# Kernel tuning notes

Measured on AMD Instinct MI355X. Metric: run time of the kernel, lower is better.

The kernel has to match this reference:

```python
import jax, jax.numpy as jnp
import numpy as np
from jax import lax

EMB, HDIM, OBS_LEN = 64, 64, 8
BATCH, NSCENES, SCENE = 32768, 4096, 8
SEQ_LEN = 12


def setup_inputs() -> dict:
    key = jax.random.key(0)
    ks = jax.random.split(key, 16)
    obs_traj = jax.random.normal(ks[0], (OBS_LEN, BATCH, 2), jnp.float32)
    last_pos = jax.random.normal(ks[1], (BATCH, 2), jnp.float32)
    last_pos_rel = jax.random.normal(ks[2], (BATCH, 2), jnp.float32)
    starts = jnp.arange(NSCENES, dtype=jnp.int32) * SCENE
    seq_start_end = jnp.stack([starts, starts + SCENE], axis=1)  # (NSCENES, 2)
    # spatial_embedding: Linear(2, EMB)
    W_se = jax.random.normal(ks[3], (EMB, 2), jnp.float32) * 0.5
    b_se = jax.random.normal(ks[4], (EMB,), jnp.float32) * 0.1
    # weight-normed convs: w = g * v / ||v||_(in,k) per out-channel, bias init zero
    def conv_params(k, cout, cin, ksz):
        ka, kb = jax.random.split(k)
        std = np.sqrt(4.0 / (ksz * cin))
        v = jax.random.normal(ka, (cout, cin, ksz), jnp.float32) * std
        g = jax.random.uniform(kb, (cout,), jnp.float32, 0.5, 1.5)
        b = jnp.zeros((cout,), jnp.float32)
        return v, g, b
    v1, g1, b1 = conv_params(ks[5], HDIM, EMB, 3)
    v2, g2, b2 = conv_params(ks[6], HDIM // 2, HDIM, 3)
    v3, g3, b3 = conv_params(ks[7], HDIM // 2, HDIM // 2, 3)
    # hidden2pos: Linear(2*HDIM, 2)
    W_hp = jax.random.normal(ks[8], (2, 2 * HDIM), jnp.float32) * 0.05
    b_hp = jax.random.normal(ks[9], (2,), jnp.float32) * 0.05
    return {"obs_traj": obs_traj, "last_pos": last_pos, "last_pos_rel": last_pos_rel,
            "W_se": W_se, "b_se": b_se,
            "v1": v1, "g1": g1, "b1": b1,
            "v2": v2, "g2": g2, "b2": b2,
            "v3": v3, "g3": g3, "b3": b3,
            "W_hp": W_hp, "b_hp": b_hp,
            "seq_start_end": seq_start_end, "seq_len": SEQ_LEN}


def _wn_conv_relu(x, v, g, b):
    # weight-norm: w[o] = g[o] * v[o] / ||v[o]||  (norm over in-channels and kernel)
    norm = jnp.sqrt(jnp.sum(v * v, axis=(1, 2)))
    w = v * (g / norm)[:, None, None]
    y = lax.conv_general_dilated(x, w, (1,), 'VALID',
                                 dimension_numbers=('NCH', 'OIH', 'NCH'))
    return jax.nn.relu(y + b[None, :, None])


def reference(obs_traj, last_pos, last_pos_rel,
              W_se, b_se, v1, g1, b1, v2, g2, b2, v3, g3, b3, W_hp, b_hp,
              seq_start_end, seq_len):
    batch = last_pos.shape[0]
    nseg = seq_start_end.shape[0]
    h_dim = v1.shape[0]
    # scene id for each pedestrian (segments are contiguous [start,end) ranges)
    seg = jnp.searchsorted(seq_start_end[:, 0], jnp.arange(batch), side='right') - 1
    # obs_traj embedding -> (batch, EMB, OBS_LEN)
    emb = obs_traj @ W_se.T + b_se            # (T, B, EMB)
    obs_emb0 = jnp.transpose(emb, (1, 2, 0))  # (B, EMB, T)

    def step(carry, _):
        obs_emb, lp = carry
        s = _wn_conv_relu(obs_emb, v1, g1, b1)   # (B, H, T-2)
        s = _wn_conv_relu(s, v2, g2, b2)         # (B, H/2, T-4)
        s = _wn_conv_relu(s, v3, g3, b3)         # (B, H/2, T-6)
        s = s.reshape(batch, h_dim)              # (H/2)*(T-6) == H
        mx = jax.ops.segment_max(s, seg, num_segments=nseg)  # ragged per-scene max
        st = jnp.concatenate([s, mx[seg]], axis=1)           # (B, 2H)
        rel = st @ W_hp.T + b_hp                 # (B, 2)
        lp = rel + lp
        dec = rel @ W_se.T + b_se                # (B, EMB)
        obs_emb = jnp.concatenate([obs_emb[:, :, 1:], dec[:, :, None]], axis=2)
        return (obs_emb, lp), rel

    _, rels = lax.scan(step, (obs_emb0, last_pos), None, length=seq_len)
    return rels  # (seq_len, batch, 2)
```

## Files before the change

kernel.cpp:

```cpp
#include <hip/hip_runtime.h>

#define BATCH 32768
#define SEQLEN 12
#define NBLK 512

typedef short short8 __attribute__((ext_vector_type(8)));
typedef float f32x4 __attribute__((ext_vector_type(4)));
typedef unsigned short ushort_t;

static __device__ __forceinline__ unsigned short f2bf(float x) {
    unsigned u = __float_as_uint(x);
    return (unsigned short)((u + 0x7FFFu + ((u >> 16) & 1u)) >> 16);
}
static __device__ __forceinline__ float bf2f(unsigned short h) {
    return __uint_as_float(((unsigned)h) << 16);
}

#define MFMA __builtin_amdgcn_mfma_f32_16x16x32_bf16


#define C1PED(PX, PY, QX, QY, RX, RY, PPED) do {                              \
    float v_ = cK1;                                                           \
    v_ = fmaf(ccA0, PX, v_); v_ = fmaf(ccB0, PY, v_);                         \
    v_ = fmaf(ccA1, QX, v_); v_ = fmaf(ccB1, QY, v_);                         \
    v_ = fmaf(ccA2, RX, v_); v_ = fmaf(ccB2, RY, v_);                         \
    v_ = fmaxf(v_, 0.f);                                                      \
    ushort_t h_ = f2bf(v_);                                                   \
    s1sh[wv][PPED][lane] = h_;                                                \
    s1sl[wv][PPED][lane] = f2bf(v_ - bf2f(h_));                               \
} while(0)

#define S1_FRAGREAD(SL) do {                                                  \
    s1fh[SL][0] = *(const short8*)&s1sh[wv][n][kg*8];                         \
    s1fh[SL][1] = *(const short8*)&s1sh[wv][n][32 + kg*8];                    \
    s1fl[SL][0] = *(const short8*)&s1sl[wv][n][kg*8];                         \
    s1fl[SL][1] = *(const short8*)&s1sl[wv][n][32 + kg*8];                    \
} while(0)

#define CONV1COL(SA, SB, SC, SL) do {                                         \
    _Pragma("unroll")                                                         \
    for (int pp_ = 0; pp_ < 8; ++pp_) {                                       \
        float4 fa_ = *(const float4*)&pos_s[wv][SA][2*pp_][0];                \
        float4 fb_ = *(const float4*)&pos_s[wv][SB][2*pp_][0];                \
        float4 fc_ = *(const float4*)&pos_s[wv][SC][2*pp_][0];                \
        C1PED(fa_.x, fa_.y, fb_.x, fb_.y, fc_.x, fc_.y, 2*pp_);               \
        C1PED(fa_.z, fa_.w, fb_.z, fb_.w, fc_.z, fc_.w, 2*pp_+1);             \
    }                                                                         \
    S1_FRAGREAD(SL);                                                          \
} while(0)

#define CONV2COL(CM3) do {                                                    \
    const float* b2b_ = &b2s[0];                                              \
    asm volatile("" : "+v"(b2b_));                                            \
    _Pragma("unroll")                                                         \
    for (int T = 0; T < 2; ++T) {                                             \
        f32x4 a1 = {0.f,0.f,0.f,0.f}, a2 = {0.f,0.f,0.f,0.f},                 \
              a3 = {0.f,0.f,0.f,0.f};                                         \
        _Pragma("unroll")                                                     \
        for (int kb = 0; kb < 6; ++kb) {                                      \
            const int sl = ((CM3) + (kb >> 1)) % 3, ich = kb & 1;             \
            const short8 wh = *(const short8*)&c2wh[T*6+kb][lane][0];         \
            const short8 wl = *(const short8*)&c2wl[T*6+kb][lane][0];         \
            a1 = MFMA(wh, s1fh[sl][ich], a1, 0, 0, 0);                        \
            a2 = MFMA(wh, s1fl[sl][ich], a2, 0, 0, 0);                        \
            a3 = MFMA(wl, s1fh[sl][ich], a3, 0, 0, 0);                        \
        }                                                                     \
        const float4 bb = *(const float4*)&b2b_[T*16 + kg*4];                 \
        float w0 = fmaxf(a1[0]+a2[0]+a3[0]+bb.x, 0.f);                        \
        float w1 = fmaxf(a1[1]+a2[1]+a3[1]+bb.y, 0.f);                        \
        float w2 = fmaxf(a1[2]+a2[2]+a3[2]+bb.z, 0.f);                        \
        float w3 = fmaxf(a1[3]+a2[3]+a3[3]+bb.w, 0.f);                        \
        ushort_t h0=f2bf(w0), h1=f2bf(w1), h2=f2bf(w2), h3=f2bf(w3);          \
        *(uint2*)&s2sh[wv][n][T*16 + kg*4] = make_uint2(                      \
            (unsigned)h0 | ((unsigned)h1 << 16),                              \
            (unsigned)h2 | ((unsigned)h3 << 16));                             \
        *(uint2*)&s2sl[wv][n][T*16 + kg*4] = make_uint2(                      \
            (unsigned)f2bf(w0-bf2f(h0)) | ((unsigned)f2bf(w1-bf2f(h1)) << 16),\
            (unsigned)f2bf(w2-bf2f(h2)) | ((unsigned)f2bf(w3-bf2f(h3)) << 16));\
    }                                                                         \
    s2fh[(CM3)] = *(const short8*)&s2sh[wv][n][kg*8];                         \
    s2fl[(CM3)] = *(const short8*)&s2sl[wv][n][kg*8];                         \
} while(0)

#define CONV3COL(VM3, PARI) do {                                              \
    const float* b3b_ = &b3s[0];                                              \
    asm volatile("" : "+v"(b3b_));                                            \
    _Pragma("unroll")                                                         \
    for (int T = 0; T < 2; ++T) {                                             \
        f32x4 a1 = {0.f,0.f,0.f,0.f}, a2 = {0.f,0.f,0.f,0.f},                 \
              a3 = {0.f,0.f,0.f,0.f};                                         \
        _Pragma("unroll")                                                     \
        for (int kb = 0; kb < 3; ++kb) {                                      \
            const int sl = ((VM3) + kb) % 3;                                  \
            const short8 wh = *(const short8*)&c3wh[T*3+kb][lane][0];         \
            a1 = MFMA(wh, s2fh[sl], a1, 0, 0, 0);                             \
            a2 = MFMA(wh, s2fl[sl], a2, 0, 0, 0);                             \
            a3 = MFMA(c3l[T][kb], s2fh[sl], a3, 0, 0, 0);                     \
        }                                                                     \
        const float4 b3v = *(const float4*)&b3b_[T*16 + kg*4];                \
        float m0 = fmaxf(a1[0]+a2[0]+a3[0]+b3v.x, 0.f);                       \
        float m1 = fmaxf(a1[1]+a2[1]+a3[1]+b3v.y, 0.f);                       \
        float m2 = fmaxf(a1[2]+a2[2]+a3[2]+b3v.z, 0.f);                       \
        float m3 = fmaxf(a1[3]+a2[3]+a3[3]+b3v.w, 0.f);                       \
        c3c[PARI][T] = (f32x4){m0, m1, m2, m3};                               \
        _Pragma("unroll")                                                     \
        for (int msk = 1; msk <= 4; msk <<= 1) {                              \
            m0 = fmaxf(m0, __shfl_xor(m0, msk));                              \
            m1 = fmaxf(m1, __shfl_xor(m1, msk));                              \
            m2 = fmaxf(m2, __shfl_xor(m2, msk));                              \
            m3 = fmaxf(m3, __shfl_xor(m3, msk));                              \
        }                                                                     \
        mxc[PARI][T] = (f32x4){m0, m1, m2, m3};                               \
    }                                                                         \
} while(0)

#define STAGE2(T0) do {                                                       \
    const int tau_ = (T0) + (lane >> 5);                                      \
    const int p_ = (lane >> 1) & 15, c_ = lane & 1;                           \
    pos_s[wv][tau_ & 3][p_][c_] =                                             \
        obs[(size_t)(tau_*BATCH + bped + p_)*2 + c_];                         \
} while(0)

#define STEP(K) do {                                                          \
    const int st = sbase + (K);                                               \
    float pv0a = 0.f, pv0b = 0.f, pv1a = 0.f, pv1b = 0.f;                     \
    {                                                                         \
        const float* wqf_ = &whp_s[kg][0];                                    \
        asm volatile("" : "+v"(wqf_));     \
        const float4* wq = (const float4*)wqf_;                               \
        _Pragma("unroll")                                                     \
        for (int q = 0; q < 16; ++q) {                                        \
            float4 ww = wq[q];                                                \
            _Pragma("unroll")                                                 \
            for (int e = 0; e < 4; ++e) {                                     \
                const int j2 = (q & 7)*4 + e;                                 \
                const int jj = j2 & 15;                                       \
                const int T = jj >> 3, r = (jj >> 1) & 3, col = jj & 1;       \
                const int par = col ? (((K)+1) & 1) : ((K) & 1);              \
                float val = (j2 < 16) ? c3c[par][T][r] : mxc[par][T][r];      \
                float wv_ = (e==0)?ww.x:(e==1)?ww.y:(e==2)?ww.z:ww.w;         \
                if (q < 8) { if (q & 1) pv0b = fmaf(wv_, val, pv0b);          \
                             else       pv0a = fmaf(wv_, val, pv0a); }        \
                else       { if (q & 1) pv1b = fmaf(wv_, val, pv1b);          \
                             else       pv1a = fmaf(wv_, val, pv1a); }        \
            }                                                                 \
        }                                                                     \
    }                                                                         \
    float pv0 = pv0a + pv0b, pv1 = pv1a + pv1b;                               \
    pv0 += __shfl_xor(pv0, 16); pv0 += __shfl_xor(pv0, 32);                   \
    pv1 += __shfl_xor(pv1, 16); pv1 += __shfl_xor(pv1, 32);                   \
    const float r0 = pv0 + bhp0, r1 = pv1 + bhp1;                             \
    if (lane < 16) {                                                          \
        float2 o; o.x = r0; o.y = r1;                                         \
        *(float2*)&out[(size_t)(st*BATCH + bped + lane)*2] = o;               \
    }                                                                         \
    if (st < SEQLEN-1) {                                                      \
        if (lane < 16) {                                                      \
            float2 o2; o2.x = r0; o2.y = r1;                                  \
            *(float2*)&pos_s[wv][st & 3][lane][0] = o2;         \
        }                                                                     \
        CONV1COL((st+2)&3, (st+3)&3, st&3, (K)%3);              \
        CONV2COL(((K)+1)%3);                                    \
        CONV3COL(((K)+2)%3, (K)&1);                             \
    }                                                                         \
} while(0)

__global__ __launch_bounds__(256, 2)
void enc_wp(const float* __restrict__ obs,
            const float* __restrict__ Wse, const float* __restrict__ bse,
            const float* __restrict__ v1, const float* __restrict__ g1, const float* __restrict__ b1,
            const float* __restrict__ v2, const float* __restrict__ g2, const float* __restrict__ b2,
            const float* __restrict__ v3, const float* __restrict__ g3, const float* __restrict__ b3,
            const float* __restrict__ Whp, const float* __restrict__ bhp,
            float* __restrict__ out)
{
    __shared__ __align__(16) ushort_t s1sh[4][16][72], s1sl[4][16][72];
    __shared__ __align__(16) ushort_t s2sh[4][16][40], s2sl[4][16][40];
    __shared__ __align__(16) float    pos_s[4][4][16][2];
    __shared__ __align__(16) float    whp_s[4][68];
    __shared__ __align__(16) ushort_t c2wh[12][64][8], c2wl[12][64][8];
    __shared__ __align__(16) ushort_t c3wh[6][64][8];
    __shared__ __align__(16) float    b2s[32], b3s[32];

    const int tid  = threadIdx.x;
    const int wv   = tid >> 6;
    const int lane = tid & 63;
    const int n    = lane & 15, kg = lane >> 4;
    const int bped = (blockIdx.x*4 + wv)*16;

    float* scr   = (float*)&s1sh[0][0][0];
    float* wse_s = scr;
    float* bse_s = scr + 128;
    float* sc2_s = scr + 192;
    float* sc3_s = scr + 224;

    if (wv == 0) {
        wse_s[lane] = Wse[lane]; wse_s[64 + lane] = Wse[64 + lane];
        bse_s[lane] = bse[lane];
        if (lane < 32) {
            b2s[lane] = b2[lane];
            const float* v = v2 + lane*192; float s = 0.f;
            for (int j = 0; j < 192; ++j) s += v[j]*v[j];
            sc2_s[lane] = g2[lane] / sqrtf(s);
        } else {
            b3s[lane-32] = b3[lane-32];
            const float* v = v3 + (lane-32)*96; float s = 0.f;
            for (int j = 0; j < 96; ++j) s += v[j]*v[j];
            sc3_s[lane-32] = g3[lane-32] / sqrtf(s);
        }
        #pragma unroll
        for (int q = 0; q < 4; ++q) {
            int d = lane >> 5, jp = lane & 31, jj = jp & 15;
            int T = jj >> 3, r = (jj >> 1) & 3, col = jj & 1;
            int off = (T*16 + q*4 + r)*2 + col + ((jp >= 16) ? 64 : 0);
            whp_s[q][lane] = Whp[d*128 + off];
        }
    }
    __syncthreads();

    if (wv == 0) {
        #pragma unroll
        for (int f = 0; f < 12; ++f) {
            const int T = f / 6, kb = f % 6;
            const int oc = T*16 + n, tap = kb >> 1, ich = kb & 1;
            const float s2s = sc2_s[oc];
            #pragma unroll
            for (int j = 0; j < 8; ++j) {
                const int ic = ich*32 + kg*8 + j;
                float w = v2[(size_t)(oc*64 + ic)*3 + tap] * s2s;
                ushort_t hb = f2bf(w);
                c2wh[f][lane][j] = hb;
                c2wl[f][lane][j] = f2bf(w - bf2f(hb));
            }
        }
    } else if (wv == 1) {
        #pragma unroll
        for (int f = 0; f < 6; ++f) {
            const int T = f / 3, kb = f % 3;
            const int oc = T*16 + n;
            const float s3s = sc3_s[oc];
            #pragma unroll
            for (int j = 0; j < 8; ++j) {
                const int ic = kg*8 + j;
                c3wh[f][lane][j] = f2bf(v3[(size_t)(oc*32 + ic)*3 + kb] * s3s);
            }
        }
    }

    float ccA0, ccA1, ccA2, ccB0, ccB1, ccB2, cK1;
    {
        const float* v = v1 + lane*192; float s = 0.f;
        for (int j = 0; j < 192; ++j) s += v[j]*v[j];
        const float sc1 = g1[lane] / sqrtf(s);
        float dA0=0,dA1=0,dA2=0,dB0=0,dB1=0,dB2=0,dC0=0,dC1=0,dC2=0;
        const float* vr = v1 + lane*192;
        #pragma unroll 4
        for (int ic = 0; ic < 64; ++ic) {
            float w0 = vr[ic*3], w1 = vr[ic*3+1], w2 = vr[ic*3+2];
            float we0 = wse_s[ic*2], we1 = wse_s[ic*2+1], be = bse_s[ic];
            dA0 = fmaf(w0, we0, dA0); dB0 = fmaf(w0, we1, dB0); dC0 = fmaf(w0, be, dC0);
            dA1 = fmaf(w1, we0, dA1); dB1 = fmaf(w1, we1, dB1); dC1 = fmaf(w1, be, dC1);
            dA2 = fmaf(w2, we0, dA2); dB2 = fmaf(w2, we1, dB2); dC2 = fmaf(w2, be, dC2);
        }
        ccA0 = sc1*dA0; ccA1 = sc1*dA1; ccA2 = sc1*dA2;
        ccB0 = sc1*dB0; ccB1 = sc1*dB1; ccB2 = sc1*dB2;
        cK1  = fmaf(sc1, (dC0 + dC1) + dC2, b1[lane]);
    }
    short8 c3l[2][3];
    #pragma unroll
    for (int T = 0; T < 2; ++T) {
        const int oc = T*16 + n;
        const float s3s = sc3_s[oc];
        #pragma unroll
        for (int kb = 0; kb < 3; ++kb) {
            #pragma unroll
            for (int j = 0; j < 8; ++j) {
                const int ic = kg*8 + j;
                float w = v3[(size_t)(oc*32 + ic)*3 + kb] * s3s;
                c3l[T][kb][j] = (short)f2bf(w - bf2f(f2bf(w)));
            }
        }
    }
    const float bhp0 = bhp[0], bhp1 = bhp[1];
    __syncthreads();

    short8 s1fh[3][2], s1fl[3][2], s2fh[3], s2fl[3];
    f32x4 c3c[2][2], mxc[2][2];

    STAGE2(0); STAGE2(2);
    CONV1COL(0, 1, 2, 0);
    CONV1COL(1, 2, 3, 1);
    STAGE2(4);
    CONV1COL(2, 3, 0, 2);
    CONV2COL(0);
    CONV1COL(3, 0, 1, 0);
    CONV2COL(1);
    STAGE2(6);
    CONV1COL(0, 1, 2, 1);
    CONV2COL(2);
    CONV3COL(0, 0);
    CONV1COL(1, 2, 3, 2);
    CONV2COL(0);
    CONV3COL(1, 1);

    #pragma unroll 1
    for (int hh = 0; hh < 2; ++hh) {
        const int sbase = hh * 6;
        STEP(0); STEP(1); STEP(2); STEP(3); STEP(4); STEP(5);
    }
}

extern "C" void kernel_launch(void* const* d_in, const int* in_sizes, int n_in,
                              void* d_out, int out_size, void* d_ws, size_t ws_size,
                              hipStream_t stream)
{
    const float* obs = (const float*)d_in[0];
    const float* Wse = (const float*)d_in[3];
    const float* bse = (const float*)d_in[4];
    const float* v1  = (const float*)d_in[5];
    const float* g1  = (const float*)d_in[6];
    const float* b1  = (const float*)d_in[7];
    const float* v2  = (const float*)d_in[8];
    const float* g2  = (const float*)d_in[9];
    const float* b2  = (const float*)d_in[10];
    const float* v3  = (const float*)d_in[11];
    const float* g3  = (const float*)d_in[12];
    const float* b3  = (const float*)d_in[13];
    const float* Whp = (const float*)d_in[14];
    const float* bhp = (const float*)d_in[15];

    enc_wp<<<NBLK, 256, 0, stream>>>(obs, Wse, bse, v1, g1, b1, v2, g2, b2,
                                     v3, g3, b3, Whp, bhp, (float*)d_out);
}
```

Measured before the change: 191.9 us.

## Compute conv1 directly in MFMA fragment layout and use DPP for segment max

```diff
diff --git a/kernel.cpp b/kernel.cpp
--- a/kernel.cpp
+++ b/kernel.cpp
@@ -18,35 +18,37 @@
 
 #define MFMA __builtin_amdgcn_mfma_f32_16x16x32_bf16
 
-
-#define C1PED(PX, PY, QX, QY, RX, RY, PPED) do {                              \
-    float v_ = cK1;                                                           \
-    v_ = fmaf(ccA0, PX, v_); v_ = fmaf(ccB0, PY, v_);                         \
-    v_ = fmaf(ccA1, QX, v_); v_ = fmaf(ccB1, QY, v_);                         \
-    v_ = fmaf(ccA2, RX, v_); v_ = fmaf(ccB2, RY, v_);                         \
-    v_ = fmaxf(v_, 0.f);                                                      \
-    ushort_t h_ = f2bf(v_);                                                   \
-    s1sh[wv][PPED][lane] = h_;                                                \
-    s1sl[wv][PPED][lane] = f2bf(v_ - bf2f(h_));                               \
-} while(0)
-
-#define S1_FRAGREAD(SL) do {                                                  \
-    s1fh[SL][0] = *(const short8*)&s1sh[wv][n][kg*8];                         \
-    s1fh[SL][1] = *(const short8*)&s1sh[wv][n][32 + kg*8];                    \
-    s1fl[SL][0] = *(const short8*)&s1sl[wv][n][kg*8];                         \
-    s1fl[SL][1] = *(const short8*)&s1sl[wv][n][32 + kg*8];                    \
-} while(0)
-
-#define CONV1COL(SA, SB, SC, SL) do {                                         \
+#define FMAXDPP(X, CTRL) \
+    fmaxf((X), __int_as_float(__builtin_amdgcn_mov_dpp(__float_as_int(X), (CTRL), 0xF, 0xF, true)))
+
+
+#define CONV1D(PA_, PB_, R0_, R1_, SL_) do {                                  \
     _Pragma("unroll")                                                         \
-    for (int pp_ = 0; pp_ < 8; ++pp_) {                                       \
-        float4 fa_ = *(const float4*)&pos_s[wv][SA][2*pp_][0];                \
-        float4 fb_ = *(const float4*)&pos_s[wv][SB][2*pp_][0];                \
-        float4 fc_ = *(const float4*)&pos_s[wv][SC][2*pp_][0];                \
-        C1PED(fa_.x, fa_.y, fb_.x, fb_.y, fc_.x, fc_.y, 2*pp_);               \
-        C1PED(fa_.z, fa_.w, fb_.z, fb_.w, fc_.z, fc_.w, 2*pp_+1);             \
-    }                                                                         \
-    S1_FRAGREAD(SL);                                                          \
+    for (int ich_ = 0; ich_ < 2; ++ich_) {                                    \
+        const int cb_ = ich_*32 + kg*8;                                       \
+        short8 sh_, sl_;                                                      \
+        _Pragma("unroll")                                                     \
+        for (int j_ = 0; j_ < 8; ++j_) {                                      \
+            float4 c0_ = *(const float4*)&c1t8[cb_ + j_][0];                  \
+            float4 c1_ = *(const float4*)&c1t8[cb_ + j_][4];                  \
+            float v_ = c1_.z;                                         \
+            v_ = fmaf(c0_.x, (PA_).x, v_); v_ = fmaf(c0_.y, (PA_).y, v_);     \
+            v_ = fmaf(c0_.z, (PB_).x, v_); v_ = fmaf(c0_.w, (PB_).y, v_);     \
+            v_ = fmaf(c1_.x, (R0_), v_);   v_ = fmaf(c1_.y, (R1_), v_);       \
+            v_ = fmaxf(v_, 0.f);                                              \
+            ushort_t h_ = f2bf(v_);                                           \
+            sh_[j_] = (short)h_;                                              \
+            sl_[j_] = (short)f2bf(v_ - bf2f(h_));                             \
+        }                                                                     \
+        s1fh[SL_][ich_] = sh_; s1fl[SL_][ich_] = sl_;                         \
+    }                                                                         \
+} while(0)
+
+#define WCONV1D(SA_, SB_, SC_, SL_) do {                                      \
+    float2 pa_ = *(const float2*)&pos_s[wv][SA_][n][0];                       \
+    float2 pb_ = *(const float2*)&pos_s[wv][SB_][n][0];                       \
+    float2 pc_ = *(const float2*)&pos_s[wv][SC_][n][0];                       \
+    CONV1D(pa_, pb_, pc_.x, pc_.y, SL_);                                      \
 } while(0)
 
 #define CONV2COL(CM3) do {                                                    \
@@ -103,13 +105,10 @@
         float m2 = fmaxf(a1[2]+a2[2]+a3[2]+b3v.z, 0.f);                       \
         float m3 = fmaxf(a1[3]+a2[3]+a3[3]+b3v.w, 0.f);                       \
         c3c[PARI][T] = (f32x4){m0, m1, m2, m3};                               \
-        _Pragma("unroll")                                                     \
-        for (int msk = 1; msk <= 4; msk <<= 1) {                              \
-            m0 = fmaxf(m0, __shfl_xor(m0, msk));                              \
-            m1 = fmaxf(m1, __shfl_xor(m1, msk));                              \
-            m2 = fmaxf(m2, __shfl_xor(m2, msk));                              \
-            m3 = fmaxf(m3, __shfl_xor(m3, msk));                              \
-        }                                                                     \
+        m0 = FMAXDPP(m0, 0xB1); m0 = FMAXDPP(m0, 0x4E); m0 = FMAXDPP(m0, 0x141);\
+        m1 = FMAXDPP(m1, 0xB1); m1 = FMAXDPP(m1, 0x4E); m1 = FMAXDPP(m1, 0x141);\
+        m2 = FMAXDPP(m2, 0xB1); m2 = FMAXDPP(m2, 0x4E); m2 = FMAXDPP(m2, 0x141);\
+        m3 = FMAXDPP(m3, 0xB1); m3 = FMAXDPP(m3, 0x4E); m3 = FMAXDPP(m3, 0x141);\
         mxc[PARI][T] = (f32x4){m0, m1, m2, m3};                               \
     }                                                                         \
 } while(0)
@@ -123,6 +122,8 @@
 
 #define STEP(K) do {                                                          \
     const int st = sbase + (K);                                               \
+    float2 c1pa = *(const float2*)&pos_s[wv][(st+2)&3][n][0];                 \
+    float2 c1pb = *(const float2*)&pos_s[wv][(st+3)&3][n][0];                 \
     float pv0a = 0.f, pv0b = 0.f, pv1a = 0.f, pv1b = 0.f;                     \
     {                                                                         \
         const float* wqf_ = &whp_s[kg][0];                                    \
@@ -159,7 +160,7 @@
             float2 o2; o2.x = r0; o2.y = r1;                                  \
             *(float2*)&pos_s[wv][st & 3][lane][0] = o2;         \
         }                                                                     \
-        CONV1COL((st+2)&3, (st+3)&3, st&3, (K)%3);              \
+        CONV1D(c1pa, c1pb, r0, r1, (K)%3);                      \
         CONV2COL(((K)+1)%3);                                    \
         CONV3COL(((K)+2)%3, (K)&1);                             \
     }                                                                         \
@@ -174,13 +175,13 @@
             const float* __restrict__ Whp, const float* __restrict__ bhp,
             float* __restrict__ out)
 {
-    __shared__ __align__(16) ushort_t s1sh[4][16][72], s1sl[4][16][72];
     __shared__ __align__(16) ushort_t s2sh[4][16][40], s2sl[4][16][40];
     __shared__ __align__(16) float    pos_s[4][4][16][2];
     __shared__ __align__(16) float    whp_s[4][68];
     __shared__ __align__(16) ushort_t c2wh[12][64][8], c2wl[12][64][8];
     __shared__ __align__(16) ushort_t c3wh[6][64][8];
     __shared__ __align__(16) float    b2s[32], b3s[32];
+    __shared__ __align__(16) float    c1t8[64][8];
 
     const int tid  = threadIdx.x;
     const int wv   = tid >> 6;
@@ -188,7 +189,7 @@
     const int n    = lane & 15, kg = lane >> 4;
     const int bped = (blockIdx.x*4 + wv)*16;
 
-    float* scr   = (float*)&s1sh[0][0][0];
+    float* scr   = (float*)&s2sh[0][0][0];
     float* wse_s = scr;
     float* bse_s = scr + 128;
     float* sc2_s = scr + 192;
@@ -219,6 +220,25 @@
     __syncthreads();
 
     if (wv == 0) {
+        const float* v = v1 + lane*192; float s = 0.f;
+        for (int j = 0; j < 192; ++j) s += v[j]*v[j];
+        const float sc1 = g1[lane] / sqrtf(s);
+        float dA0=0,dA1=0,dA2=0,dB0=0,dB1=0,dB2=0,dC0=0,dC1=0,dC2=0;
+        const float* vr = v1 + lane*192;
+        #pragma unroll 4
+        for (int ic = 0; ic < 64; ++ic) {
+            float w0 = vr[ic*3], w1 = vr[ic*3+1], w2 = vr[ic*3+2];
+            float we0 = wse_s[ic*2], we1 = wse_s[ic*2+1], be = bse_s[ic];
+            dA0 = fmaf(w0, we0, dA0); dB0 = fmaf(w0, we1, dB0); dC0 = fmaf(w0, be, dC0);
+            dA1 = fmaf(w1, we0, dA1); dB1 = fmaf(w1, we1, dB1); dC1 = fmaf(w1, be, dC1);
+            dA2 = fmaf(w2, we0, dA2); dB2 = fmaf(w2, we1, dB2); dC2 = fmaf(w2, be, dC2);
+        }
+        c1t8[lane][0] = sc1*dA0; c1t8[lane][1] = sc1*dB0;
+        c1t8[lane][2] = sc1*dA1; c1t8[lane][3] = sc1*dB1;
+        c1t8[lane][4] = sc1*dA2; c1t8[lane][5] = sc1*dB2;
+        c1t8[lane][6] = fmaf(sc1, (dC0 + dC1) + dC2, b1[lane]);
+        c1t8[lane][7] = 0.f;
+    } else if (wv == 2) {
         #pragma unroll
         for (int f = 0; f < 12; ++f) {
             const int T = f / 6, kb = f % 6;
@@ -245,26 +265,6 @@
                 c3wh[f][lane][j] = f2bf(v3[(size_t)(oc*32 + ic)*3 + kb] * s3s);
             }
         }
-    }
-
-    float ccA0, ccA1, ccA2, ccB0, ccB1, ccB2, cK1;
-    {
-        const float* v = v1 + lane*192; float s = 0.f;
-        for (int j = 0; j < 192; ++j) s += v[j]*v[j];
-        const float sc1 = g1[lane] / sqrtf(s);
-        float dA0=0,dA1=0,dA2=0,dB0=0,dB1=0,dB2=0,dC0=0,dC1=0,dC2=0;
-        const float* vr = v1 + lane*192;
-        #pragma unroll 4
-        for (int ic = 0; ic < 64; ++ic) {
-            float w0 = vr[ic*3], w1 = vr[ic*3+1], w2 = vr[ic*3+2];
-            float we0 = wse_s[ic*2], we1 = wse_s[ic*2+1], be = bse_s[ic];
-            dA0 = fmaf(w0, we0, dA0); dB0 = fmaf(w0, we1, dB0); dC0 = fmaf(w0, be, dC0);
-            dA1 = fmaf(w1, we0, dA1); dB1 = fmaf(w1, we1, dB1); dC1 = fmaf(w1, be, dC1);
-            dA2 = fmaf(w2, we0, dA2); dB2 = fmaf(w2, we1, dB2); dC2 = fmaf(w2, be, dC2);
-        }
-        ccA0 = sc1*dA0; ccA1 = sc1*dA1; ccA2 = sc1*dA2;
-        ccB0 = sc1*dB0; ccB1 = sc1*dB1; ccB2 = sc1*dB2;
-        cK1  = fmaf(sc1, (dC0 + dC1) + dC2, b1[lane]);
     }
     short8 c3l[2][3];
     #pragma unroll
@@ -288,18 +288,18 @@
     f32x4 c3c[2][2], mxc[2][2];
 
     STAGE2(0); STAGE2(2);
-    CONV1COL(0, 1, 2, 0);
-    CONV1COL(1, 2, 3, 1);
+    WCONV1D(0, 1, 2, 0);
+    WCONV1D(1, 2, 3, 1);
     STAGE2(4);
-    CONV1COL(2, 3, 0, 2);
+    WCONV1D(2, 3, 0, 2);
     CONV2COL(0);
-    CONV1COL(3, 0, 1, 0);
+    WCONV1D(3, 0, 1, 0);
     CONV2COL(1);
     STAGE2(6);
-    CONV1COL(0, 1, 2, 1);
+    WCONV1D(0, 1, 2, 1);
     CONV2COL(2);
     CONV3COL(0, 0);
-    CONV1COL(1, 2, 3, 2);
+    WCONV1D(1, 2, 3, 2);
     CONV2COL(0);
     CONV3COL(1, 1);
 
```

New measurement: 176.6 us. -8.0%, faster.
